# Kernel tuning notes

Hardware: AMD Instinct MI355X
Metric: run time of the kernel (lower is better)

Reference implementation:

```python
import jax, jax.numpy as jnp
import numpy as np
import math

B, L, D = 4, 4096, 1024
D_EMB, D_HID = 3, 16


def make_pos_emb(emb_dim, seq_len):
    # Complex exponential positional embeddings (non-trainable), shape (1, seq_len, emb_dim)
    t = np.linspace(0.0, 1.0, seq_len, dtype=np.float32)[None, :, None]
    bands = (emb_dim - 1) // 2
    t_res = np.linspace(0.0, seq_len - 1, seq_len, dtype=np.float32)[None, :, None]
    w = 2.0 * math.pi * t_res / seq_len
    f = np.linspace(0.0001, max(bands - 1, 0), bands, dtype=np.float32)[None, None]
    z = np.exp(-1j * (f * w).astype(np.complex64))
    z = np.concatenate([t, z.real.astype(np.float32), z.imag.astype(np.float32)], axis=-1)
    return jnp.asarray(z)


def setup_inputs() -> dict:
    key = jax.random.key(0)
    ks = jax.random.split(key, 8)
    u = jax.random.normal(ks[0], (B, L, D), dtype=jnp.float32)
    z = make_pos_emb(D_EMB, L)  # (1, L, D_EMB)
    # filter MLP: Linear(d_emb, d_hidden) -> ReLU -> Linear(d_hidden, d_model)
    s1 = 1.0 / math.sqrt(D_EMB)
    w1 = jax.random.uniform(ks[1], (D_HID, D_EMB), jnp.float32, -s1, s1)
    b1 = jax.random.uniform(ks[2], (D_HID,), jnp.float32, -s1, s1)
    s2 = 1.0 / math.sqrt(D_HID)
    w2 = jax.random.uniform(ks[3], (D, D_HID), jnp.float32, -s2, s2)
    b2 = jax.random.uniform(ks[4], (D,), jnp.float32, -s2, s2)
    # projection: Linear(d_model, d_model)
    sp = 1.0 / math.sqrt(D)
    pw = jax.random.uniform(ks[5], (D, D), jnp.float32, -sp, sp)
    pb = jax.random.uniform(ks[6], (D,), jnp.float32, -sp, sp)
    return {"u": u, "z": z, "w1": w1, "b1": b1, "w2": w2, "b2": b2, "pw": pw, "pb": pb}


def fft_conv(u_bdl, k_dl):
    # u_bdl: (B, D, L), k_dl: (1, D, L) or (D, L)
    seqlen = u_bdl.shape[-1]
    fft_size = 2 * seqlen
    k_f = jnp.fft.rfft(k_dl, n=fft_size) / fft_size
    u_f = jnp.fft.rfft(u_bdl, n=fft_size)
    y = jnp.fft.irfft(u_f * k_f, n=fft_size, norm="forward")[..., :seqlen]
    return y


def reference(u, z, w1, b1, w2, b2, pw, pb):
    seqlen = u.shape[1]
    pe = z[:, :seqlen]  # (1, L, D_EMB)
    h = jax.nn.relu(jnp.einsum("ble,he->blh", pe, w1) + b1)
    filt = jnp.einsum("blh,dh->bld", h, w2) + b2  # (1, L, D)
    filt = jnp.transpose(filt, (0, 2, 1))  # (1, D, L)
    u_conv = fft_conv(jnp.transpose(u, (0, 2, 1)), filt)  # (B, D, L)
    u_conv = jnp.transpose(u_conv, (0, 2, 1)).astype(u.dtype)  # (B, L, D)
    u_proj = jnp.einsum("bld,od->blo", u, pw) + pb
    return u_conv * u_proj + u
```

## Files before the change

### kernel.cpp

```cpp
#include <hip/hip_runtime.h>
#include <hip/hip_bf16.h>

#define SEQL 4096
#define DCH  1024
#define BATCH 4
#define KH   4097

typedef float2 cf;
__device__ __forceinline__ cf mkc(float x, float y){ return make_float2(x,y); }
__device__ __forceinline__ cf cadd(cf a, cf b){ return mkc(a.x+b.x, a.y+b.y); }
__device__ __forceinline__ cf csub(cf a, cf b){ return mkc(a.x-b.x, a.y-b.y); }
__device__ __forceinline__ cf cmul(cf a, cf b){ return mkc(a.x*b.x - a.y*b.y, a.x*b.y + a.y*b.x); }
__device__ __forceinline__ cf cconjf(cf a){ return mkc(a.x, -a.y); }
__device__ __forceinline__ cf addi(cf a, cf b){ return mkc(a.x - b.y, a.y + b.x); }
__device__ __forceinline__ cf subi(cf a, cf b){ return mkc(a.x + b.y, a.y - b.x); }
__device__ __forceinline__ int cpad(int i){ return i + (i >> 4); }
__device__ __forceinline__ int drev(int i){
    return ((i>>10)&3) | (((i>>8)&3)<<2) | (((i>>6)&3)<<4)
         | (((i>>4)&3)<<6) | (((i>>2)&3)<<8) | ((i&3)<<10);
}

__device__ __forceinline__ cf W1c(int j){
    const float cs[4] = {1.f, 0.92387953f, 0.70710678f, 0.38268343f};
    const float sn[4] = {0.f, -0.38268343f, -0.70710678f, -0.92387953f};
    return mkc(cs[j], sn[j]);
}
__device__ __forceinline__ cf W2c(int j){
    const float cs[4] = {1.f, 0.70710678f, 0.f, -0.70710678f};
    const float sn[4] = {0.f, -0.70710678f, -1.f, -0.70710678f};
    return mkc(cs[j], sn[j]);
}
__device__ __forceinline__ cf W3c(int j){
    const float cs[4] = {1.f, 0.38268343f, -0.70710678f, -0.92387953f};
    const float sn[4] = {0.f, -0.92387953f, -0.70710678f, 0.38268343f};
    return mkc(cs[j], sn[j]);
}

__device__ __forceinline__ unsigned pack2bf(float a, float b){
    unsigned r;
    asm("v_cvt_pk_bf16_f32 %0, %1, %2" : "=v"(r) : "v"(a), "v"(b));
    return r;
}
__device__ __forceinline__ float bflo(unsigned u){ return __uint_as_float(u << 16); }
__device__ __forceinline__ float bfhi(unsigned u){ return __uint_as_float(u & 0xffff0000u); }

__global__ __launch_bounds__(256) void twiddle_init(cf* __restrict__ tw4, cf* __restrict__ tw8){
    int i = blockIdx.x*256 + threadIdx.x;
    const double TWO_PI = 6.283185307179586476925286766559;
    double a4 = -TWO_PI * (double)i / 4096.0;
    double a8 = -TWO_PI * (double)i / 8192.0;
    tw4[i] = mkc((float)cos(a4), (float)sin(a4));
    tw8[i] = mkc((float)cos(a8), (float)sin(a8));
}

__global__ __launch_bounds__(256) void mlp_kernel(
        const float* __restrict__ z, const float* __restrict__ w1,
        const float* __restrict__ b1, float* __restrict__ h) {
    int l = blockIdx.x * blockDim.x + threadIdx.x;
    if (l >= SEQL) return;
    float pe0 = z[l * 3 + 0], pe1 = z[l * 3 + 1], pe2 = z[l * 3 + 2];
#pragma unroll
    for (int j = 0; j < 16; ++j) {
        float v = pe0 * w1[j * 3 + 0] + pe1 * w1[j * 3 + 1] + pe2 * w1[j * 3 + 2] + b1[j];
        h[l * 16 + j] = v > 0.f ? v : 0.f;
    }
}

__global__ __launch_bounds__(256) void transpose_kernel(
        const float* __restrict__ u, float* __restrict__ ut) {
    __shared__ float tile[32][33];
    int b = blockIdx.z;
    int l0 = blockIdx.x * 32;
    int d0 = blockIdx.y * 32;
    int tx = threadIdx.x, ty = threadIdx.y;
    const float* up = u + (size_t)b * SEQL * DCH;
#pragma unroll
    for (int i = 0; i < 32; i += 8)
        tile[ty + i][tx] = up[(size_t)(l0 + ty + i) * DCH + d0 + tx];
    __syncthreads();
    float* utp = ut + (size_t)b * DCH * SEQL;
#pragma unroll
    for (int i = 0; i < 32; i += 8)
        utp[(size_t)(d0 + ty + i) * SEQL + l0 + tx] = tile[tx][ty + i];
}

__device__ void dif_mid_and_chunk(cf* lds, const cf* __restrict__ tw){
    const int tid = threadIdx.x;
#pragma unroll
    for (int p = 1; p < 4; ++p) {
        const int lm = 10 - 2*p;
        const int m  = 1 << lm;
        const int step = 1024 >> lm;
#pragma unroll
        for (int it = 0; it < 4; ++it) {
            int j = tid + (it << 8);
            int k = j & (m-1);
            int g = j >> lm;
            int i0 = (g << (lm+2)) + k;
            cf x0 = lds[cpad(i0)];
            cf x1 = lds[cpad(i0+m)];
            cf x2 = lds[cpad(i0+2*m)];
            cf x3 = lds[cpad(i0+3*m)];
            cf b0 = cadd(x0,x2), b1 = csub(x0,x2);
            cf b2 = cadd(x1,x3), b3 = csub(x1,x3);
            cf u0 = cadd(b0,b2);
            cf u2 = csub(b0,b2);
            cf u1 = subi(b1,b3);
            cf u3 = addi(b1,b3);
            int t1 = k*step;
            lds[cpad(i0)]     = u0;
            lds[cpad(i0+m)]   = cmul(u1, tw[t1]);
            lds[cpad(i0+2*m)] = cmul(u2, tw[2*t1]);
            lds[cpad(i0+3*m)] = cmul(u3, tw[3*t1]);
        }
        __syncthreads();
    }
    {
        int base = 17*tid;
        cf v[16];
#pragma unroll
        for (int j=0;j<16;++j) v[j] = lds[base+j];
#pragma unroll
        for (int j=0;j<4;++j){
            cf x0=v[j], x1=v[j+4], x2=v[j+8], x3=v[j+12];
            cf b0=cadd(x0,x2), b1=csub(x0,x2), b2=cadd(x1,x3), b3=csub(x1,x3);
            cf u0=cadd(b0,b2), u2=csub(b0,b2), u1=subi(b1,b3), u3=addi(b1,b3);
            v[j]    = u0;
            v[j+4]  = cmul(u1, W1c(j));
            v[j+8]  = cmul(u2, W2c(j));
            v[j+12] = cmul(u3, W3c(j));
        }
#pragma unroll
        for (int c=0;c<4;++c){
            cf x0=v[4*c], x1=v[4*c+1], x2=v[4*c+2], x3=v[4*c+3];
            cf b0=cadd(x0,x2), b1=csub(x0,x2), b2=cadd(x1,x3), b3=csub(x1,x3);
            v[4*c]   = cadd(b0,b2);
            v[4*c+1] = subi(b1,b3);
            v[4*c+2] = csub(b0,b2);
            v[4*c+3] = addi(b1,b3);
        }
#pragma unroll
        for (int j=0;j<16;++j) lds[base+j] = v[j];
        __syncthreads();
    }
}

__device__ void dit_chunk_and_mid(cf* lds, const cf* __restrict__ tw){
    const int tid = threadIdx.x;
    {
        int base = 17*tid;
        cf v[16];
#pragma unroll
        for (int j=0;j<16;++j) v[j] = lds[base+j];
#pragma unroll
        for (int c=0;c<4;++c){
            cf a0=v[4*c], a1=v[4*c+1], a2=v[4*c+2], a3=v[4*c+3];
            cf b0=cadd(a0,a2), b1=csub(a0,a2), b2=cadd(a1,a3), b3=csub(a1,a3);
            v[4*c]   = cadd(b0,b2);
            v[4*c+1] = addi(b1,b3);
            v[4*c+2] = csub(b0,b2);
            v[4*c+3] = subi(b1,b3);
        }
#pragma unroll
        for (int j=0;j<4;++j){
            cf a0=v[j];
            cf a1=cmul(v[j+4],  cconjf(W1c(j)));
            cf a2=cmul(v[j+8],  cconjf(W2c(j)));
            cf a3=cmul(v[j+12], cconjf(W3c(j)));
            cf b0=cadd(a0,a2), b1=csub(a0,a2), b2=cadd(a1,a3), b3=csub(a1,a3);
            v[j]    = cadd(b0,b2);
            v[j+4]  = addi(b1,b3);
            v[j+8]  = csub(b0,b2);
            v[j+12] = subi(b1,b3);
        }
#pragma unroll
        for (int j=0;j<16;++j) lds[base+j] = v[j];
        __syncthreads();
    }
#pragma unroll
    for (int p = 0; p < 3; ++p) {
        const int lm = 4 + 2*p;
        const int m  = 1 << lm;
        const int step = 1024 >> lm;
#pragma unroll
        for (int it = 0; it < 4; ++it) {
            int j = tid + (it << 8);
            int k = j & (m-1);
            int g = j >> lm;
            int i0 = (g << (lm+2)) + k;
            int t1 = k*step;
            cf a0 = lds[cpad(i0)];
            cf a1 = cmul(lds[cpad(i0+m)],   cconjf(tw[t1]));
            cf a2 = cmul(lds[cpad(i0+2*m)], cconjf(tw[2*t1]));
            cf a3 = cmul(lds[cpad(i0+3*m)], cconjf(tw[3*t1]));
            cf b0=cadd(a0,a2), b1=csub(a0,a2), b2=cadd(a1,a3), b3=csub(a1,a3);
            lds[cpad(i0)]     = cadd(b0,b2);
            lds[cpad(i0+m)]   = addi(b1,b3);
            lds[cpad(i0+2*m)] = csub(b0,b2);
            lds[cpad(i0+3*m)] = subi(b1,b3);
        }
        __syncthreads();
    }
}

__global__ __launch_bounds__(256) void filt_fft_kernel(
        const float* __restrict__ h, const float* __restrict__ w2,
        const float* __restrict__ b2, const cf* __restrict__ tw4,
        const cf* __restrict__ tw8, cf* __restrict__ kf) {
    __shared__ cf lds[4352];
    const int d = blockIdx.x;
    const int tid = threadIdx.x;
    float wv[16];
#pragma unroll
    for (int j = 0; j < 16; ++j) wv[j] = w2[d * 16 + j];
    const float bb = b2[d];
#pragma unroll
    for (int it = 0; it < 4; ++it) {
        int j = tid + (it << 8);
        const float* h0 = h + (size_t)(2*j) * 16;
        const float* h1 = h + (size_t)(2*(j+1024)) * 16;
        float f0 = bb, f1 = bb, f2 = bb, f3 = bb;
#pragma unroll
        for (int i = 0; i < 16; ++i) {
            f0 += h0[i] * wv[i];  f1 += h0[16+i] * wv[i];
            f2 += h1[i] * wv[i];  f3 += h1[16+i] * wv[i];
        }
        cf x0 = mkc(f0, f1), x1 = mkc(f2, f3);
        cf u0 = cadd(x0,x1);
        cf u2 = csub(x0,x1);
        cf u1 = subi(x0,x1);
        cf u3 = addi(x0,x1);
        lds[cpad(j)]      = u0;
        lds[cpad(j+1024)] = cmul(u1, tw4[j]);
        lds[cpad(j+2048)] = cmul(u2, tw4[2*j]);
        lds[cpad(j+3072)] = cmul(u3, tw4[3*j]);
    }
    __syncthreads();
    dif_mid_and_chunk(lds, tw4);
    const float s = 1.f / 8192.f;
    cf* Hrow = kf + (size_t)d * KH;
    const int lane  = tid & 63;
    const int kbase = ((lane & 31) << 6) | ((lane >> 5) << 5) | ((tid >> 6) << 3);
#pragma unroll
    for (int it = 0; it < 8; ++it) {
        int k = kbase + it;
        if (k == 0) {
            cf c0 = lds[cpad(0)];
            Hrow[0]    = mkc((c0.x + c0.y) * s, 0.f);
            Hrow[4096] = mkc((c0.x - c0.y) * s, 0.f);
            cf c2 = lds[cpad(drev(2048))];
            Hrow[2048] = mkc(c2.x * s, -c2.y * s);
        } else {
            int kk = 4096 - k;
            cf ck  = lds[cpad(drev(k))];
            cf ckk = lds[cpad(drev(kk))];
            cf cc = cconjf(ckk);
            cf E  = mkc(0.5f*(ck.x+cc.x), 0.5f*(ck.y+cc.y));
            cf Dd = csub(ck, cc);
            cf O  = mkc(0.5f*Dd.y, -0.5f*Dd.x);
            cf wvv = tw8[k];
            cf Xk  = cadd(E, cmul(wvv, O));
            cf wp  = mkc(-wvv.x, wvv.y);
            cf Xkk = cadd(cconjf(E), cmul(wp, cconjf(O)));
            Hrow[k]  = mkc(Xk.x * s, Xk.y * s);
            Hrow[kk] = mkc(Xkk.x * s, Xkk.y * s);
        }
    }
}

__global__ __launch_bounds__(256) void conv_kernel(
        float* __restrict__ uty, const cf* __restrict__ tw4,
        const cf* __restrict__ tw8, const cf* __restrict__ kf) {
    __shared__ cf lds[4352];
    const int row = blockIdx.x;
    const int d = row & (DCH - 1);
    const int tid = threadIdx.x;
    float* rp = uty + (size_t)row * SEQL;
#pragma unroll
    for (int it = 0; it < 4; ++it) {
        int j = tid + (it << 8);
        cf x0 = *(const cf*)&rp[2*j];
        cf x1 = *(const cf*)&rp[2*(j+1024)];
        cf u0 = cadd(x0,x1);
        cf u2 = csub(x0,x1);
        cf u1 = subi(x0,x1);
        cf u3 = addi(x0,x1);
        lds[cpad(j)]      = u0;
        lds[cpad(j+1024)] = cmul(u1, tw4[j]);
        lds[cpad(j+2048)] = cmul(u2, tw4[2*j]);
        lds[cpad(j+3072)] = cmul(u3, tw4[3*j]);
    }
    __syncthreads();
    dif_mid_and_chunk(lds, tw4);
    const cf* Hrow = kf + (size_t)d * KH;
    {
        const int lane  = tid & 63;
        const int kbase = ((lane & 31) << 6) | ((lane >> 5) << 5) | ((tid >> 6) << 3);
#pragma unroll
        for (int it = 0; it < 8; ++it) {
            int k = kbase + it;
            if (k == 0) {
                cf c0 = lds[cpad(0)];
                float X0 = c0.x + c0.y, X4 = c0.x - c0.y;
                cf H0 = Hrow[0], H4 = Hrow[4096];
                cf Y0 = mkc(X0 * H0.x, X0 * H0.y);
                cf Y4 = mkc(X4 * H4.x, X4 * H4.y);
                cf S  = cadd(Y0, Y4), Dd = csub(Y0, Y4);
                lds[cpad(0)] = addi(S, Dd);
                int s2 = cpad(drev(2048));
                cf c2 = lds[s2];
                cf Y2 = cmul(cconjf(c2), Hrow[2048]);
                lds[s2] = mkc(2.f * Y2.x, -2.f * Y2.y);
            } else {
                int kk = 4096 - k;
                int sk = cpad(drev(k)), skk = cpad(drev(kk));
                cf ck = lds[sk], ckk = lds[skk];
                cf cc = cconjf(ckk);
                cf E  = mkc(0.5f*(ck.x+cc.x), 0.5f*(ck.y+cc.y));
                cf Dd = csub(ck, cc);
                cf O  = mkc(0.5f*Dd.y, -0.5f*Dd.x);
                cf wv = tw8[k];
                cf Xk  = cadd(E, cmul(wv, O));
                cf wp  = mkc(-wv.x, wv.y);
                cf Xkk = cadd(cconjf(E), cmul(wp, cconjf(O)));
                cf Yk  = cmul(Xk,  Hrow[k]);
                cf Ykk = cmul(Xkk, Hrow[kk]);
                cf cy = cconjf(Ykk);
                cf S  = cadd(Yk, cy), D2 = csub(Yk, cy);
                cf Zk = addi(S, cmul(cconjf(wv), D2));
                cf cy2 = cconjf(Yk);
                cf S2  = cadd(Ykk, cy2), D3 = csub(Ykk, cy2);
                cf Zkk = subi(S2, cmul(wv, D3));
                lds[sk] = Zk; lds[skk] = Zkk;
            }
        }
    }
    __syncthreads();
    dit_chunk_and_mid(lds, tw4);
    unsigned short* yb = (unsigned short*)rp;
#pragma unroll
    for (int it = 0; it < 4; ++it) {
        int j = tid + (it << 8);
        cf a0 = lds[cpad(j)];
        cf a1 = cmul(lds[cpad(j+1024)], cconjf(tw4[j]));
        cf a2 = cmul(lds[cpad(j+2048)], cconjf(tw4[2*j]));
        cf a3 = cmul(lds[cpad(j+3072)], cconjf(tw4[3*j]));
        cf b0 = cadd(a0,a2), b1 = csub(a0,a2);
        cf b2 = cadd(a1,a3), b3 = csub(a1,a3);
        cf o0 = cadd(b0,b2);
        cf o1 = addi(b1,b3);
        *(unsigned*)&yb[2*j]          = pack2bf(o0.x, o0.y);
        *(unsigned*)&yb[2*(j+1024)]   = pack2bf(o1.x, o1.y);
    }
}

typedef __attribute__((ext_vector_type(8))) short short8;
typedef __attribute__((ext_vector_type(4))) float f32x4;

__global__ __launch_bounds__(256, 3) void gemm_mfma_kernel(
        const float* __restrict__ u, const float* __restrict__ pw,
        const float* __restrict__ pb, const unsigned short* __restrict__ yb,
        float* __restrict__ out) {
    __shared__ char lds_raw[34816];
    float (*ysc)[132] = (float(*)[132])lds_raw;

    const int tid  = threadIdx.x;
    const int lane = tid & 63;
    const int wid  = tid >> 6;
    const int wr   = wid >> 1;
    const int wc   = wid & 1;
    const int m0   = blockIdx.x * 128;
    const int n0   = blockIdx.y * 128;

    f32x4 acc[4][4] = {};
    float4 ra[4], rb[4];

    int s_row[4], s_f4[4];
#pragma unroll
    for (int j = 0; j < 4; ++j) {
        int idx = j * 256 + tid;
        s_row[j] = idx >> 3;
        s_f4[j]  = idx & 7;
    }

#define LOADT(kt)                                                                     \
    {                                                                                 \
        _Pragma("unroll")                                                             \
        for (int j = 0; j < 4; ++j) {                                                 \
            ra[j] = *(const float4*)&u [(size_t)(m0 + s_row[j]) * DCH + (kt) + s_f4[j] * 4]; \
            rb[j] = *(const float4*)&pw[(size_t)(n0 + s_row[j]) * DCH + (kt) + s_f4[j] * 4]; \
        }                                                                             \
    }
#define WRITET(base)                                                                  \
    {                                                                                 \
        _Pragma("unroll")                                                             \
        for (int j = 0; j < 4; ++j) {                                                 \
            int off = (base) + ((s_row[j] * 64 + s_f4[j] * 8) ^ ((s_row[j] & 3) << 4)); \
            uint2 pa, pbv2;                                                           \
            pa.x   = pack2bf(ra[j].x, ra[j].y);  pa.y   = pack2bf(ra[j].z, ra[j].w);  \
            pbv2.x = pack2bf(rb[j].x, rb[j].y);  pbv2.y = pack2bf(rb[j].z, rb[j].w);  \
            *(uint2*)(lds_raw + off)        = pa;                                     \
            *(uint2*)(lds_raw + off + 8192) = pbv2;                                   \
        }                                                                             \
    }

    LOADT(0);
    WRITET(0);
    LOADT(32);
    __syncthreads();

    for (int t = 0; t < 32; ++t) {
        const int cur = (t & 1) << 14;
        short8 af[4], bf[4];
#pragma unroll
        for (int f = 0; f < 4; ++f) {
            int rowA = wr * 64 + f * 16 + (lane & 15);
            int rowB = wc * 64 + f * 16 + (lane & 15);
            int offA = cur + ((rowA * 64 + ((lane >> 4) * 16)) ^ ((rowA & 3) << 4));
            int offB = cur + 8192 + ((rowB * 64 + ((lane >> 4) * 16)) ^ ((rowB & 3) << 4));
            af[f] = *(short8*)(lds_raw + offA);
            bf[f] = *(short8*)(lds_raw + offB);
        }
        if (t < 31) WRITET(cur ^ 16384);
        if (t < 30) LOADT((t + 2) * 32);
#pragma unroll
        for (int mf = 0; mf < 4; ++mf)
#pragma unroll
            for (int nf = 0; nf < 4; ++nf)
                acc[mf][nf] = __builtin_amdgcn_mfma_f32_16x16x32_bf16(
                    af[mf], bf[nf], acc[mf][nf], 0, 0, 0);
        __syncthreads();
    }

    const int b  = m0 >> 12;
    const int l0 = m0 & (SEQL - 1);
    float pbv[4];
#pragma unroll
    for (int nf = 0; nf < 4; ++nf)
        pbv[nf] = pb[n0 + wc * 64 + nf * 16 + (lane & 15)];

    for (int c = 0; c < 2; ++c) {
        __syncthreads();
#pragma unroll
        for (int j = 0; j < 4; ++j) {
            int idx = j * 256 + tid;
            int dn  = idx >> 3;
            int lg  = idx & 7;
            uint4 w4 = *(const uint4*)&yb[(((size_t)(b * DCH + n0 + dn)) << 13) + l0 + c * 64 + lg * 8];
            int lb = lg * 8;
            ysc[lb+0][dn] = bflo(w4.x); ysc[lb+1][dn] = bfhi(w4.x);
            ysc[lb+2][dn] = bflo(w4.y); ysc[lb+3][dn] = bfhi(w4.y);
            ysc[lb+4][dn] = bflo(w4.z); ysc[lb+5][dn] = bfhi(w4.z);
            ysc[lb+6][dn] = bflo(w4.w); ysc[lb+7][dn] = bfhi(w4.w);
        }
        __syncthreads();
        if (wr == c) {
#pragma unroll
            for (int mf = 0; mf < 4; ++mf)
#pragma unroll
                for (int i = 0; i < 4; ++i) {
                    int lrow = mf * 16 + (lane >> 4) * 4 + i;
                    int m = m0 + c * 64 + lrow;
#pragma unroll
                    for (int nf = 0; nf < 4; ++nf) {
                        int nl = wc * 64 + nf * 16 + (lane & 15);
                        int n = n0 + nl;
                        float proj = acc[mf][nf][i] + pbv[nf];
                        out[(size_t)m * DCH + n] = ysc[lrow][nl] * proj + u[(size_t)m * DCH + n];
                    }
                }
        }
    }
#undef LOADT
#undef WRITET
}

extern "C" void kernel_launch(void* const* d_in, const int* in_sizes, int n_in,
                              void* d_out, int out_size, void* d_ws, size_t ws_size,
                              hipStream_t stream) {
    const float* u  = (const float*)d_in[0];
    const float* z  = (const float*)d_in[1];
    const float* w1 = (const float*)d_in[2];
    const float* b1 = (const float*)d_in[3];
    const float* w2 = (const float*)d_in[4];
    const float* b2 = (const float*)d_in[5];
    const float* pw = (const float*)d_in[6];
    const float* pb = (const float*)d_in[7];
    float* out = (float*)d_out;

    float* h   = (float*)d_ws;
    float* uty = (float*)((char*)d_ws + 262144);
    cf* kf  = (cf*)d_out;
    cf* tw4 = (cf*)((char*)d_out + (40u << 20));
    cf* tw8 = tw4 + 4096;

    twiddle_init<<<dim3(16), dim3(256), 0, stream>>>(tw4, tw8);
    mlp_kernel<<<dim3(16), dim3(256), 0, stream>>>(z, w1, b1, h);
    transpose_kernel<<<dim3(SEQL / 32, DCH / 32, BATCH), dim3(32, 8), 0, stream>>>(u, uty);
    filt_fft_kernel<<<dim3(DCH), dim3(256), 0, stream>>>(h, w2, b2, tw4, tw8, kf);
    conv_kernel<<<dim3(BATCH * DCH), dim3(256), 0, stream>>>(uty, tw4, tw8, kf);
    gemm_mfma_kernel<<<dim3(128, 8), dim3(256), 0, stream>>>(u, pw, pb, (const unsigned short*)uty, out);
}
```

Measured before the change: 285.2 us.

## Pre-convert GEMM operands to bf16 and stage tiles with direct global-to-LDS loads

The transpose kernel now also writes a bf16 copy of u, and a new kernel converts pw to bf16 in workspace. A new GEMM reads those bf16 operands with global_load_lds 16-byte transfers into swizzled, double-buffered LDS tiles. This removes the per-tile fp32 register loads and bf16 packing, and halves operand bytes across the repeated tile reads. The cost is extra conversion traffic and workspace, a fallback path used when workspace is too small, and a residual add that now uses bf16 u instead of fp32 u, which lowers accuracy.

```diff
diff --git a/kernel.cpp b/kernel.cpp
--- a/kernel.cpp
+++ b/kernel.cpp
@@ -44,6 +44,11 @@
 __device__ __forceinline__ float bflo(unsigned u){ return __uint_as_float(u << 16); }
 __device__ __forceinline__ float bfhi(unsigned u){ return __uint_as_float(u & 0xffff0000u); }
 
+__device__ __forceinline__ void gload16(const void* g, void* l){
+    __builtin_amdgcn_global_load_lds((const __attribute__((address_space(1))) void*)g,
+                                     (__attribute__((address_space(3))) void*)l, 16, 0, 0);
+}
+
 __global__ __launch_bounds__(256) void twiddle_init(cf* __restrict__ tw4, cf* __restrict__ tw8){
     int i = blockIdx.x*256 + threadIdx.x;
     const double TWO_PI = 6.283185307179586476925286766559;
@@ -67,21 +72,38 @@
 }
 
 __global__ __launch_bounds__(256) void transpose_kernel(
-        const float* __restrict__ u, float* __restrict__ ut) {
+        const float* __restrict__ u, float* __restrict__ ut,
+        unsigned short* __restrict__ ub) {
     __shared__ float tile[32][33];
     int b = blockIdx.z;
     int l0 = blockIdx.x * 32;
     int d0 = blockIdx.y * 32;
     int tx = threadIdx.x, ty = threadIdx.y;
     const float* up = u + (size_t)b * SEQL * DCH;
-#pragma unroll
-    for (int i = 0; i < 32; i += 8)
-        tile[ty + i][tx] = up[(size_t)(l0 + ty + i) * DCH + d0 + tx];
+    unsigned short* ubp = ub ? ub + (size_t)b * SEQL * DCH : (unsigned short*)0;
+#pragma unroll
+    for (int i = 0; i < 32; i += 8) {
+        size_t idx = (size_t)(l0 + ty + i) * DCH + d0 + tx;
+        float v = up[idx];
+        tile[ty + i][tx] = v;
+        if (ub) ubp[idx] = (unsigned short)pack2bf(v, v);
+    }
     __syncthreads();
     float* utp = ut + (size_t)b * DCH * SEQL;
 #pragma unroll
     for (int i = 0; i < 32; i += 8)
         utp[(size_t)(d0 + ty + i) * SEQL + l0 + tx] = tile[tx][ty + i];
+}
+
+__global__ __launch_bounds__(256) void pw2bf_kernel(
+        const float* __restrict__ pw, unsigned short* __restrict__ pwb) {
+    int t = blockIdx.x * 256 + threadIdx.x;
+    float4 a = *(const float4*)&pw[(size_t)t * 8];
+    float4 b = *(const float4*)&pw[(size_t)t * 8 + 4];
+    uint4 o;
+    o.x = pack2bf(a.x, a.y); o.y = pack2bf(a.z, a.w);
+    o.z = pack2bf(b.x, b.y); o.w = pack2bf(b.z, b.w);
+    *(uint4*)&pwb[(size_t)t * 8] = o;
 }
 
 __device__ void dif_mid_and_chunk(cf* lds, const cf* __restrict__ tw){
@@ -357,8 +379,8 @@
 typedef __attribute__((ext_vector_type(8))) short short8;
 typedef __attribute__((ext_vector_type(4))) float f32x4;
 
-__global__ __launch_bounds__(256, 3) void gemm_mfma_kernel(
-        const float* __restrict__ u, const float* __restrict__ pw,
+__global__ __launch_bounds__(256, 4) void gemm_mfma_v2(
+        const unsigned short* __restrict__ ub, const unsigned short* __restrict__ pwb,
         const float* __restrict__ pb, const unsigned short* __restrict__ yb,
         float* __restrict__ out) {
     __shared__ char lds_raw[34816];
@@ -373,8 +395,105 @@
     const int n0   = blockIdx.y * 128;
 
     f32x4 acc[4][4] = {};
+
+    const int srow = lane >> 2;
+    const int scol = 16 * ((lane & 3) ^ ((lane >> 2) & 3));
+
+#define STAGE2(bufbase, kt)                                                                   \
+    {                                                                                         \
+        _Pragma("unroll")                                                                     \
+        for (int i = 0; i < 2; ++i) {                                                         \
+            int c = wid * 2 + i;                                                              \
+            const char* gA = (const char*)ub  + (size_t)(m0 + c * 16 + srow) * 2048 + (kt) * 2 + scol; \
+            const char* gB = (const char*)pwb + (size_t)(n0 + c * 16 + srow) * 2048 + (kt) * 2 + scol; \
+            gload16(gA, lds_raw + (bufbase) + c * 1024);                                      \
+            gload16(gB, lds_raw + (bufbase) + 8192 + c * 1024);                               \
+        }                                                                                     \
+    }
+
+    STAGE2(0, 0);
+    __syncthreads();
+
+    for (int t = 0; t < 32; ++t) {
+        const int cur = (t & 1) << 14;
+        if (t < 31) STAGE2(cur ^ 16384, (t + 1) * 32);
+        short8 af[4], bfr[4];
+#pragma unroll
+        for (int f = 0; f < 4; ++f) {
+            int rowA = wr * 64 + f * 16 + (lane & 15);
+            int rowB = wc * 64 + f * 16 + (lane & 15);
+            int offA = cur + rowA * 64 + (((lane >> 4) * 16) ^ ((rowA & 3) << 4));
+            int offB = cur + 8192 + rowB * 64 + (((lane >> 4) * 16) ^ ((rowB & 3) << 4));
+            af[f]  = *(short8*)(lds_raw + offA);
+            bfr[f] = *(short8*)(lds_raw + offB);
+        }
+#pragma unroll
+        for (int mf = 0; mf < 4; ++mf)
+#pragma unroll
+            for (int nf = 0; nf < 4; ++nf)
+                acc[mf][nf] = __builtin_amdgcn_mfma_f32_16x16x32_bf16(
+                    af[mf], bfr[nf], acc[mf][nf], 0, 0, 0);
+        __syncthreads();
+    }
+
+    const int b  = m0 >> 12;
+    const int l0 = m0 & (SEQL - 1);
+    float pbv[4];
+#pragma unroll
+    for (int nf = 0; nf < 4; ++nf)
+        pbv[nf] = pb[n0 + wc * 64 + nf * 16 + (lane & 15)];
+
+    for (int c = 0; c < 2; ++c) {
+        __syncthreads();
+#pragma unroll
+        for (int j = 0; j < 4; ++j) {
+            int idx = j * 256 + tid;
+            int dn  = idx >> 3;
+            int lg  = idx & 7;
+            uint4 w4 = *(const uint4*)&yb[(((size_t)(b * DCH + n0 + dn)) << 13) + l0 + c * 64 + lg * 8];
+            int lb = lg * 8;
+            ysc[lb+0][dn] = bflo(w4.x); ysc[lb+1][dn] = bfhi(w4.x);
+            ysc[lb+2][dn] = bflo(w4.y); ysc[lb+3][dn] = bfhi(w4.y);
+            ysc[lb+4][dn] = bflo(w4.z); ysc[lb+5][dn] = bfhi(w4.z);
+            ysc[lb+6][dn] = bflo(w4.w); ysc[lb+7][dn] = bfhi(w4.w);
+        }
+        __syncthreads();
+        if (wr == c) {
+#pragma unroll
+            for (int mf = 0; mf < 4; ++mf)
+#pragma unroll
+                for (int i = 0; i < 4; ++i) {
+                    int lrow = mf * 16 + (lane >> 4) * 4 + i;
+                    int m = m0 + c * 64 + lrow;
+#pragma unroll
+                    for (int nf = 0; nf < 4; ++nf) {
+                        int nl = wc * 64 + nf * 16 + (lane & 15);
+                        int n = n0 + nl;
+                        float proj = acc[mf][nf][i] + pbv[nf];
+                        float ures = __uint_as_float((unsigned)ub[(size_t)m * DCH + n] << 16);
+                        out[(size_t)m * DCH + n] = ysc[lrow][nl] * proj + ures;
+                    }
+                }
+        }
+    }
+#undef STAGE2
+}
+
+__global__ __launch_bounds__(256, 3) void gemm_mfma_fb(
+        const float* __restrict__ u, const float* __restrict__ pw,
+        const float* __restrict__ pb, const unsigned short* __restrict__ yb,
+        float* __restrict__ out) {
+    __shared__ char lds_raw[34816];
+    float (*ysc)[132] = (float(*)[132])lds_raw;
+    const int tid  = threadIdx.x;
+    const int lane = tid & 63;
+    const int wid  = tid >> 6;
+    const int wr   = wid >> 1;
+    const int wc   = wid & 1;
+    const int m0   = blockIdx.x * 128;
+    const int n0   = blockIdx.y * 128;
+    f32x4 acc[4][4] = {};
     float4 ra[4], rb[4];
-
     int s_row[4], s_f4[4];
 #pragma unroll
     for (int j = 0; j < 4; ++j) {
@@ -382,7 +501,6 @@
         s_row[j] = idx >> 3;
         s_f4[j]  = idx & 7;
     }
-
 #define LOADT(kt)                                                                     \
     {                                                                                 \
         _Pragma("unroll")                                                             \
@@ -403,23 +521,21 @@
             *(uint2*)(lds_raw + off + 8192) = pbv2;                                   \
         }                                                                             \
     }
-
     LOADT(0);
     WRITET(0);
     LOADT(32);
     __syncthreads();
-
     for (int t = 0; t < 32; ++t) {
         const int cur = (t & 1) << 14;
-        short8 af[4], bf[4];
+        short8 af[4], bfr[4];
 #pragma unroll
         for (int f = 0; f < 4; ++f) {
             int rowA = wr * 64 + f * 16 + (lane & 15);
             int rowB = wc * 64 + f * 16 + (lane & 15);
             int offA = cur + ((rowA * 64 + ((lane >> 4) * 16)) ^ ((rowA & 3) << 4));
             int offB = cur + 8192 + ((rowB * 64 + ((lane >> 4) * 16)) ^ ((rowB & 3) << 4));
-            af[f] = *(short8*)(lds_raw + offA);
-            bf[f] = *(short8*)(lds_raw + offB);
+            af[f]  = *(short8*)(lds_raw + offA);
+            bfr[f] = *(short8*)(lds_raw + offB);
         }
         if (t < 31) WRITET(cur ^ 16384);
         if (t < 30) LOADT((t + 2) * 32);
@@ -428,17 +544,15 @@
 #pragma unroll
             for (int nf = 0; nf < 4; ++nf)
                 acc[mf][nf] = __builtin_amdgcn_mfma_f32_16x16x32_bf16(
-                    af[mf], bf[nf], acc[mf][nf], 0, 0, 0);
-        __syncthreads();
-    }
-
+                    af[mf], bfr[nf], acc[mf][nf], 0, 0, 0);
+        __syncthreads();
+    }
     const int b  = m0 >> 12;
     const int l0 = m0 & (SEQL - 1);
     float pbv[4];
 #pragma unroll
     for (int nf = 0; nf < 4; ++nf)
         pbv[nf] = pb[n0 + wc * 64 + nf * 16 + (lane & 15)];
-
     for (int c = 0; c < 2; ++c) {
         __syncthreads();
 #pragma unroll
@@ -490,14 +604,27 @@
 
     float* h   = (float*)d_ws;
     float* uty = (float*)((char*)d_ws + 262144);
-    cf* kf  = (cf*)d_out;
-    cf* tw4 = (cf*)((char*)d_out + (40u << 20));
+    cf* kf = (cf*)d_out;
+
+    const size_t ub_off  = 262144 + (size_t)BATCH * DCH * SEQL * sizeof(float);
+    const size_t pwb_off = ub_off + (size_t)BATCH * SEQL * DCH * sizeof(unsigned short);
+    const size_t tw_off  = pwb_off + (size_t)DCH * DCH * sizeof(unsigned short);
+    const size_t need    = tw_off + 2 * 4096 * sizeof(cf);
+    const bool   big     = ws_size >= need;
+
+    cf* tw4 = big ? (cf*)((char*)d_ws + tw_off) : (cf*)((char*)d_out + (40u << 20));
     cf* tw8 = tw4 + 4096;
+    unsigned short* ub  = big ? (unsigned short*)((char*)d_ws + ub_off)  : (unsigned short*)0;
+    unsigned short* pwb = big ? (unsigned short*)((char*)d_ws + pwb_off) : (unsigned short*)0;
 
     twiddle_init<<<dim3(16), dim3(256), 0, stream>>>(tw4, tw8);
     mlp_kernel<<<dim3(16), dim3(256), 0, stream>>>(z, w1, b1, h);
-    transpose_kernel<<<dim3(SEQL / 32, DCH / 32, BATCH), dim3(32, 8), 0, stream>>>(u, uty);
+    transpose_kernel<<<dim3(SEQL / 32, DCH / 32, BATCH), dim3(32, 8), 0, stream>>>(u, uty, ub);
+    if (big) pw2bf_kernel<<<dim3(512), dim3(256), 0, stream>>>(pw, pwb);
     filt_fft_kernel<<<dim3(DCH), dim3(256), 0, stream>>>(h, w2, b2, tw4, tw8, kf);
     conv_kernel<<<dim3(BATCH * DCH), dim3(256), 0, stream>>>(uty, tw4, tw8, kf);
-    gemm_mfma_kernel<<<dim3(128, 8), dim3(256), 0, stream>>>(u, pw, pb, (const unsigned short*)uty, out);
-}
+    if (big)
+        gemm_mfma_v2<<<dim3(128, 8), dim3(256), 0, stream>>>(ub, pwb, pb, (const unsigned short*)uty, out);
+    else
+        gemm_mfma_fb<<<dim3(128, 8), dim3(256), 0, stream>>>(u, pw, pb, (const unsigned short*)uty, out);
+}
```

New measurement: 275.6 us. 3.4% less time.
